# Kernel tuning notes

Measured on AMD Instinct MI355X. Metric: run time of the kernel, lower is better.

## Reference

```python
import jax, jax.numpy as jnp
import numpy as np

EMB = 2048
NQH = 16          # num_q_heads
G = 4             # group_size
NKV = NQH // G    # 4 kv heads
HD = EMB // NQH   # 128 head_dim
B, S = 2, 2048


def setup_inputs() -> dict:
    key = jax.random.key(0)
    ks = jax.random.split(key, 6)
    scale = 1.0 / np.sqrt(EMB)
    x = jax.random.normal(ks[0], (B, S, EMB), dtype=jnp.float32)
    attn_mask = jnp.zeros((B, S), dtype=bool)  # unused placeholder
    # torch Linear weights: (out_features, in_features)
    Wq = jax.random.normal(ks[1], (EMB, EMB), dtype=jnp.float32) * scale
    Wk = jax.random.normal(ks[2], (EMB // G, EMB), dtype=jnp.float32) * scale
    Wv = jax.random.normal(ks[3], (EMB // G, EMB), dtype=jnp.float32) * scale
    Wo = jax.random.normal(ks[4], (EMB, EMB), dtype=jnp.float32) * scale
    return {"x": x, "attn_mask": attn_mask, "is_causal": 1,
            "Wq": Wq, "Wk": Wk, "Wv": Wv, "Wo": Wo}


def reference(x, attn_mask, is_causal, Wq, Wk, Wv, Wo):
    b, n, _ = x.shape
    q = x @ Wq.T                      # (b, n, EMB)
    k = x @ Wk.T                      # (b, n, EMB//G)
    v = x @ Wv.T                      # (b, n, EMB//G)
    # q: b n (h_full d) -> b h_full n d, then (h g) split with h=NKV outer
    q = q.reshape(b, n, NQH, HD).transpose(0, 2, 1, 3)      # (b, NQH, n, d)
    q = q.reshape(b, NKV, G, n, HD).transpose(0, 2, 1, 3, 4)  # (b, g, h, n, d)
    k = k.reshape(b, n, NKV, HD).transpose(0, 2, 1, 3)      # (b, h, s, d)
    v = v.reshape(b, n, NKV, HD).transpose(0, 2, 1, 3)      # (b, h, s, d)
    attn = jnp.einsum('bghnd,bhsd->bghns', q, k) / np.sqrt(HD)
    scores = jax.nn.softmax(attn, axis=-1)  # dropout p=0.0 -> identity
    out = jnp.einsum('bghns,bhsd->bghnd', scores, v)        # (b, g, h, n, d)
    # b g h n d -> b n (h g) d -> b n (h g d)
    out = out.transpose(0, 3, 2, 1, 4).reshape(b, n, EMB)
    y = out @ Wo.T
    return y
```

## Files before the change

kernel.cpp:

```cpp
#include <hip/hip_runtime.h>
#include <stdint.h>


typedef short s8v __attribute__((ext_vector_type(8)));
typedef float f4  __attribute__((ext_vector_type(4)));
typedef unsigned short u16;

#define GLD_LDS(g, l) __builtin_amdgcn_global_load_lds(                     \
    (const __attribute__((address_space(1))) void*)(g),                     \
    (__attribute__((address_space(3))) void*)(l), 16, 0, 0)

__device__ __forceinline__ u16 f2bf(float f) {
    union { float f; uint32_t u; } v; v.f = f;
    uint32_t u = v.u;
    return (u16)((u + 0x7fffu + ((u >> 16) & 1u)) >> 16);
}

__device__ __forceinline__ float fexp2(float x) {
#if __has_builtin(__builtin_amdgcn_exp2f)
    return __builtin_amdgcn_exp2f(x);
#else
    return exp2f(x);
#endif
}

__global__ void cvt_all(const float* __restrict__ x,  const float* __restrict__ wq,
                        const float* __restrict__ wk, const float* __restrict__ wv,
                        const float* __restrict__ wo_,
                        u16* __restrict__ xb, u16* __restrict__ wqkv,
                        u16* __restrict__ wob)
{
    int i = blockIdx.x * blockDim.x + threadIdx.x;
    const float4* s; ushort4* d; int so, dofs;
    if (i < 2097152)      { s = (const float4*)x;   d = (ushort4*)xb;   so = i;           dofs = so; }
    else if (i < 3145728) { s = (const float4*)wq;  d = (ushort4*)wqkv; so = i - 2097152; dofs = so; }
    else if (i < 3407872) { s = (const float4*)wk;  d = (ushort4*)wqkv; so = i - 3145728; dofs = so + 1048576; }
    else if (i < 3670016) { s = (const float4*)wv;  d = (ushort4*)wqkv; so = i - 3407872; dofs = so + 1310720; }
    else                  { s = (const float4*)wo_; d = (ushort4*)wob;  so = i - 3670016; dofs = so; }
    float4 v = s[so];
    ushort4 o;
    o.x = f2bf(v.x); o.y = f2bf(v.y); o.z = f2bf(v.z); o.w = f2bf(v.w);
    d[dofs] = o;
}

__global__ __launch_bounds__(512, 1)
void gemm256x192(const u16* __restrict__ A, const u16* __restrict__ Bm,
                 int K,
                 u16* __restrict__ qkOut, u16* __restrict__ vtOut)
{
    __shared__ __attribute__((aligned(16))) u16 ldsA[2][2][8192];
    __shared__ __attribute__((aligned(16))) u16 ldsB[2][12288];

    const int tid  = threadIdx.x;
    const int lane = tid & 63, quad = lane >> 4, l16 = lane & 15;
    const int wave = tid >> 6;
    const int wr = wave >> 2, wc = wave & 3;

    int bx, by;
    {
        const int nwgx = gridDim.x;
        const int nwg  = nwgx * gridDim.y;
        const int flat = blockIdx.y * nwgx + blockIdx.x;
        const int nflat = (flat & 7) * (nwg >> 3) + (flat >> 3);
        bx = nflat % nwgx; by = nflat / nwgx;
    }
    const int m0 = by * 256, n0 = bx * 192;
    const int NT = K >> 6;

    f4 acc[8][3] = {};

#define VMC3() asm volatile("s_waitcnt vmcnt(3)" ::: "memory")
#define VMC0() asm volatile("s_waitcnt vmcnt(0)" ::: "memory")
#define BAR()  __builtin_amdgcn_s_barrier()

#define STGA(bf, h, t) if ((t) < NT) {                                      \
        _Pragma("unroll")                                                   \
        for (int j = 0; j < 2; j++) {                                       \
            int s_ = j * 512 + tid;                                         \
            int r_ = s_ >> 3, cc = s_ & 7;                                  \
            GLD_LDS(A + (size_t)(m0 + (h) * 128 + r_) * K + (t) * 64        \
                      + ((cc ^ (r_ & 7)) << 3),                             \
                    &ldsA[bf][h][(j * 512 + (tid & ~63)) * 8]);             \
        } }

#define STGB(bf, t) if ((t) < NT) {                                         \
        _Pragma("unroll")                                                   \
        for (int j = 0; j < 3; j++) {                                       \
            int s_ = j * 512 + tid;                                         \
            int r_ = s_ >> 3, cc = s_ & 7;                                  \
            GLD_LDS(Bm + (size_t)(n0 + r_) * K + (t) * 64                   \
                       + ((cc ^ (r_ & 7)) << 3),                            \
                    &ldsB[bf][(j * 512 + (tid & ~63)) * 8]);                \
        } }

#define RD_A(bf, qm, ar) {                                                  \
        _Pragma("unroll")                                                   \
        for (int f = 0; f < 4; f++) {                                       \
            int r_ = (qm) * 64 + f * 16 + l16;                              \
            _Pragma("unroll")                                               \
            for (int kc = 0; kc < 2; kc++)                                  \
                ar[f][kc] = *(const s8v*)(&ldsA[bf][wr]                     \
                    [r_ * 64 + (((kc * 4 + quad) ^ (r_ & 7)) << 3)]);       \
        } }

#define RD_B(bf, br) {                                                      \
        _Pragma("unroll")                                                   \
        for (int f = 0; f < 3; f++) {                                       \
            int r_ = wc * 48 + f * 16 + l16;                                \
            _Pragma("unroll")                                               \
            for (int kc = 0; kc < 2; kc++)                                  \
                br[f][kc] = *(const s8v*)(&ldsB[bf]                         \
                    [r_ * 64 + (((kc * 4 + quad) ^ (r_ & 7)) << 3)]);       \
        } }

#define MM(qm, ar, br) {                                                    \
        __builtin_amdgcn_s_setprio(1);                                      \
        _Pragma("unroll")                                                   \
        for (int f = 0; f < 4; f++)                                         \
            _Pragma("unroll")                                               \
            for (int g = 0; g < 3; g++) {                                   \
                acc[(qm)*4+f][g] = __builtin_amdgcn_mfma_f32_16x16x32_bf16( \
                    ar[f][0], br[g][0], acc[(qm)*4+f][g], 0, 0, 0);         \
                acc[(qm)*4+f][g] = __builtin_amdgcn_mfma_f32_16x16x32_bf16( \
                    ar[f][1], br[g][1], acc[(qm)*4+f][g], 0, 0, 0);         \
            }                                                               \
        __builtin_amdgcn_s_setprio(0); }

    STGA(0,0,0); STGA(0,1,0); STGB(0,0);
    STGB(1,1);
    VMC3(); BAR();

    for (int T = 0; T < NT; T += 2) {
        const bool more = (T + 2 < NT);
        s8v a0[4][2], a1[4][2], b[3][2];
        RD_A(0,0,a0); RD_B(0,b);
        STGA(1,0,T+1); STGA(1,1,T+1);
        BAR(); MM(0,a0,b); BAR();
        RD_A(0,1,a1);
        STGB(0,T+2);
        BAR(); MM(1,a1,b);
        if (more) { VMC3(); } else { VMC0(); }
        BAR();
        RD_A(1,0,a0); RD_B(1,b);
        STGA(0,0,T+2); STGA(0,1,T+2);
        BAR(); MM(0,a0,b); BAR();
        RD_A(1,1,a1);
        STGB(1,T+3);
        BAR(); MM(1,a1,b);
        if (more) { VMC3(); } else { VMC0(); }
        BAR();
    }
#undef STGA
#undef STGB
#undef RD_A
#undef RD_B
#undef MM
#undef VMC3
#undef VMC0
#undef BAR

    const float qs = 0.08838834764831845f * 1.4426950408889634f;
    #pragma unroll
    for (int mi = 0; mi < 8; mi++) {
        int gm0 = m0 + wr * 128 + mi * 16 + quad * 4;
        int bb = gm0 >> 11, s = gm0 & 2047;
        #pragma unroll
        for (int ni = 0; ni < 3; ni++) {
            int base = n0 + wc * 48 + ni * 16;
            int gn = base + l16;
            if (base < 2048) {
                #pragma unroll
                for (int r = 0; r < 4; r++)
                    qkOut[(size_t)(gm0 + r) * 2560 + gn] = f2bf(acc[mi][ni][r] * qs);
            } else if (base < 2560) {
                #pragma unroll
                for (int r = 0; r < 4; r++)
                    qkOut[(size_t)(gm0 + r) * 2560 + gn] = f2bf(acc[mi][ni][r]);
            } else {
                int dd = gn - 2560;
                ushort4 pk;
                pk.x = f2bf(acc[mi][ni][0]); pk.y = f2bf(acc[mi][ni][1]);
                pk.z = f2bf(acc[mi][ni][2]); pk.w = f2bf(acc[mi][ni][3]);
                *(ushort4*)(vtOut +
                    ((size_t)(bb * 4 + (dd >> 7)) * 128 + (dd & 127)) * 2048 + s) = pk;
            }
        }
    }
}

__global__ __launch_bounds__(512, 1)
void gemm256x128(const u16* __restrict__ A, const u16* __restrict__ Bm,
                 int M, int N, int K, float* __restrict__ fOut)
{
    __shared__ __attribute__((aligned(16))) u16 lds[2][3][8192];

    const int tid  = threadIdx.x;
    const int lane = tid & 63, quad = lane >> 4, l16 = lane & 15;
    const int wave = tid >> 6;
    const int wr = wave >> 2, wc = wave & 3;

    int bx, by;
    {
        const int nwgx = gridDim.x;
        const int nwg  = nwgx * gridDim.y;
        const int flat = blockIdx.y * nwgx + blockIdx.x;
        const int nflat = (flat & 7) * (nwg >> 3) + (flat >> 3);
        bx = nflat % nwgx; by = nflat / nwgx;
    }
    const int m0 = by * 256, n0 = bx * 128;
    const int NT = K >> 6;

    f4 acc[8][2] = {};

#define VMC2() asm volatile("s_waitcnt vmcnt(2)" ::: "memory")
#define VMC0() asm volatile("s_waitcnt vmcnt(0)" ::: "memory")
#define BAR()  __builtin_amdgcn_s_barrier()

#define STG(bf, u, t) if ((t) < NT) {                                       \
        const u16* gb = ((u) == 2) ? Bm : A;                                \
        const int rb = ((u) == 2) ? n0 : (m0 + (u) * 128);                  \
        _Pragma("unroll")                                                   \
        for (int j = 0; j < 2; j++) {                                       \
            int s_ = j * 512 + tid;                                         \
            int r_ = s_ >> 3, cc = s_ & 7;                                  \
            GLD_LDS(gb + (size_t)(rb + r_) * K + (t) * 64                   \
                       + ((cc ^ (r_ & 7)) << 3),                            \
                    &lds[bf][u][(j * 512 + (tid & ~63)) * 8]);              \
        } }

#define RD_A(bf, qm, ar) {                                                  \
        _Pragma("unroll")                                                   \
        for (int f = 0; f < 4; f++) {                                       \
            int r_ = (qm) * 64 + f * 16 + l16;                              \
            _Pragma("unroll")                                               \
            for (int kc = 0; kc < 2; kc++)                                  \
                ar[f][kc] = *(const s8v*)(&lds[bf][wr]                      \
                    [r_ * 64 + (((kc * 4 + quad) ^ (r_ & 7)) << 3)]);       \
        } }

#define RD_B(bf, br) {                                                      \
        _Pragma("unroll")                                                   \
        for (int f = 0; f < 2; f++) {                                       \
            int r_ = wc * 32 + f * 16 + l16;                                \
            _Pragma("unroll")                                               \
            for (int kc = 0; kc < 2; kc++)                                  \
                br[f][kc] = *(const s8v*)(&lds[bf][2]                       \
                    [r_ * 64 + (((kc * 4 + quad) ^ (r_ & 7)) << 3)]);       \
        } }

#define MM(qm, ar, br) {                                                    \
        __builtin_amdgcn_s_setprio(1);                                      \
        _Pragma("unroll")                                                   \
        for (int f = 0; f < 4; f++)                                         \
            _Pragma("unroll")                                               \
            for (int g = 0; g < 2; g++) {                                   \
                acc[(qm)*4+f][g] = __builtin_amdgcn_mfma_f32_16x16x32_bf16( \
                    ar[f][0], br[g][0], acc[(qm)*4+f][g], 0, 0, 0);         \
                acc[(qm)*4+f][g] = __builtin_amdgcn_mfma_f32_16x16x32_bf16( \
                    ar[f][1], br[g][1], acc[(qm)*4+f][g], 0, 0, 0);         \
            }                                                               \
        __builtin_amdgcn_s_setprio(0); }

    STG(0,0,0); STG(0,1,0); STG(0,2,0);
    STG(1,2,1);
    VMC2(); BAR();

    for (int T = 0; T < NT; T += 2) {
        const bool more = (T + 2 < NT);
        s8v a0[4][2], a1[4][2], b[2][2];
        RD_A(0,0,a0); RD_B(0,b);
        STG(1,0,T+1); STG(1,1,T+1);
        BAR(); MM(0,a0,b); BAR();
        RD_A(0,1,a1);
        STG(0,2,T+2);
        BAR(); MM(1,a1,b);
        if (more) { VMC2(); } else { VMC0(); }
        BAR();
        RD_A(1,0,a0); RD_B(1,b);
        STG(0,0,T+2); STG(0,1,T+2);
        BAR(); MM(0,a0,b); BAR();
        RD_A(1,1,a1);
        STG(1,2,T+3);
        BAR(); MM(1,a1,b);
        if (more) { VMC2(); } else { VMC0(); }
        BAR();
    }
#undef STG
#undef RD_A
#undef RD_B
#undef MM
#undef VMC2
#undef VMC0
#undef BAR

    #pragma unroll
    for (int mi = 0; mi < 8; mi++) {
        int gm0 = m0 + wr * 128 + mi * 16 + quad * 4;
        #pragma unroll
        for (int ni = 0; ni < 2; ni++) {
            int gn = n0 + wc * 32 + ni * 16 + l16;
            #pragma unroll
            for (int r = 0; r < 4; r++)
                fOut[(size_t)(gm0 + r) * N + gn] = acc[mi][ni][r];
        }
    }
}

__global__ __launch_bounds__(512, 1)
void attn_kernel(const u16* __restrict__ qk, const u16* __restrict__ vt,
                 u16* __restrict__ ao)
{
    __shared__ __attribute__((aligned(16))) u16 Kb[3][64 * 128];
    __shared__ __attribute__((aligned(16))) u16 Vb[3][128 * 64];
    __shared__ __attribute__((aligned(16))) u16 Ps[8][32 * 72];

    const int tid  = threadIdx.x;
    const int wave = tid >> 6, lane = tid & 63;
    const int quad = lane >> 4, l16 = lane & 15;
    const int bh = blockIdx.x;
    const int b = bh >> 2, h = bh & 3;
    const int hh = wave >> 1, mh = wave & 1;
    const int hq = h * 4 + hh;
    const int qs0 = blockIdx.y * 64;

    s8v aq[2][4];
    #pragma unroll
    for (int mt = 0; mt < 2; mt++) {
        const u16* qrow = qk + (size_t)(b * 2048 + qs0 + (mh * 2 + mt) * 16 + l16) * 2560
                             + hq * 128 + quad * 8;
        #pragma unroll
        for (int c4 = 0; c4 < 4; c4++) aq[mt][c4] = *(const s8v*)(qrow + c4 * 32);
    }

    s8v ones;
    #pragma unroll
    for (int j = 0; j < 8; j++) ones[j] = (short)0x3F80;

    f4 o[2][9] = {};

    const u16* kbase = qk + (size_t)(b * 2048) * 2560 + 2048 + h * 128;
    const u16* vbase = vt + (size_t)bh * 128 * 2048;
    u16* Pw = &Ps[wave][0];

    int bkb[4], bvb[2];
    #pragma unroll
    for (int c4 = 0; c4 < 4; c4++)
        bkb[c4] = l16 * 128 + (((c4 * 4 + quad) ^ (l16 & 7)) * 8);
    #pragma unroll
    for (int kc = 0; kc < 2; kc++)
        bvb[kc] = l16 * 64 + (((kc * 4 + quad) ^ (l16 & 7)) * 8);
    const int apb = l16 * 72 + quad * 8;
    const int psw = l16 * 72 + quad * 4;

#define VMC4() asm volatile("s_waitcnt vmcnt(4)" ::: "memory")
#define VMC0() asm volatile("s_waitcnt vmcnt(0)" ::: "memory")

#define STAGE(BUF, S) {                                                       \
        _Pragma("unroll")                                                     \
        for (int i = 0; i < 2; i++) {                                         \
            const int c = wave + i * 8;                                       \
            int kr = c * 4 + (lane >> 4);                                     \
            int ksw = (lane & 15) ^ (kr & 7);                                 \
            GLD_LDS(kbase + (size_t)((S) + kr) * 2560 + ksw * 8,              \
                    &Kb[BUF][c * 512]);                                       \
            int vd = c * 8 + (lane >> 3);                                     \
            int vsw = (lane & 7) ^ (vd & 7);                                  \
            GLD_LDS(vbase + (size_t)vd * 2048 + (S) + vsw * 8,                \
                    &Vb[BUF][c * 512]);                                       \
        } }

#define STEP(CUR, NXT, S) {                                                   \
        if ((S) + 64 < 2048) { VMC4(); } else { VMC0(); }                     \
        __builtin_amdgcn_s_barrier();                                         \
        if ((S) + 128 < 2048) STAGE(NXT, (S) + 128);                          \
        s8v bk[4][4];                                                         \
        _Pragma("unroll")                                                     \
        for (int c4 = 0; c4 < 4; c4++)                                        \
            _Pragma("unroll")                                                 \
            for (int cg = 0; cg < 4; cg++)                                    \
                bk[c4][cg] = *(const s8v*)(&Kb[CUR][bkb[c4] + cg * 2048]);    \
        _Pragma("unroll")                                                     \
        for (int mt = 0; mt < 2; mt++) {                                      \
            f4 sc[4] = {};                                                    \
            _Pragma("unroll")                                                 \
            for (int c4 = 0; c4 < 4; c4++)                                    \
                _Pragma("unroll")                                             \
                for (int cg = 0; cg < 4; cg++)                                \
                    sc[cg] = __builtin_amdgcn_mfma_f32_16x16x32_bf16(         \
                        bk[c4][cg], aq[mt][c4], sc[cg], 0, 0, 0);             \
            _Pragma("unroll")                                                 \
            for (int cg = 0; cg < 4; cg++) {                                  \
                ushort4 pk;                                                   \
                pk.x = (u16)(__float_as_uint(fexp2(sc[cg][0])) >> 16);        \
                pk.y = (u16)(__float_as_uint(fexp2(sc[cg][1])) >> 16);        \
                pk.z = (u16)(__float_as_uint(fexp2(sc[cg][2])) >> 16);        \
                pk.w = (u16)(__float_as_uint(fexp2(sc[cg][3])) >> 16);        \
                *(ushort4*)(Pw + psw + mt * 1152 + cg * 16) = pk;             \
            }                                                                 \
        }                                                                     \
        s8v ap[2][2];                                                         \
        _Pragma("unroll")                                                     \
        for (int mt = 0; mt < 2; mt++)                                        \
            _Pragma("unroll")                                                 \
            for (int kc = 0; kc < 2; kc++)                                    \
                ap[mt][kc] = *(const s8v*)(Pw + apb + mt * 1152 + kc * 32);   \
        _Pragma("unroll")                                                     \
        for (int ch = 0; ch < 8; ch++) {                                      \
            s8v bv0 = *(const s8v*)(&Vb[CUR][bvb[0] + ch * 1024]);            \
            s8v bv1 = *(const s8v*)(&Vb[CUR][bvb[1] + ch * 1024]);            \
            _Pragma("unroll")                                                 \
            for (int mt = 0; mt < 2; mt++) {                                  \
                o[mt][ch] = __builtin_amdgcn_mfma_f32_16x16x32_bf16(          \
                    ap[mt][0], bv0, o[mt][ch], 0, 0, 0);                      \
                o[mt][ch] = __builtin_amdgcn_mfma_f32_16x16x32_bf16(          \
                    ap[mt][1], bv1, o[mt][ch], 0, 0, 0);                      \
            }                                                                 \
        }                                                                     \
        _Pragma("unroll")                                                     \
        for (int mt = 0; mt < 2; mt++) {                                      \
            o[mt][8] = __builtin_amdgcn_mfma_f32_16x16x32_bf16(               \
                ap[mt][0], ones, o[mt][8], 0, 0, 0);                          \
            o[mt][8] = __builtin_amdgcn_mfma_f32_16x16x32_bf16(               \
                ap[mt][1], ones, o[mt][8], 0, 0, 0);                          \
        } }

    STAGE(0, 0);
    STAGE(1, 64);
    int s0 = 0;
    for (int it = 0; it < 10; ++it, s0 += 192) {
        STEP(0, 2, s0);
        STEP(1, 0, s0 + 64);
        STEP(2, 1, s0 + 128);
    }
    STEP(0, 2, 1920);
    STEP(1, 0, 1984);
#undef STEP
#undef STAGE
#undef VMC4
#undef VMC0

    #pragma unroll
    for (int mt = 0; mt < 2; mt++)
        #pragma unroll
        for (int r = 0; r < 4; r++) {
            float inv = 1.f / o[mt][8][r];
            int gm = b * 2048 + qs0 + (mh * 2 + mt) * 16 + quad * 4 + r;
            #pragma unroll
            for (int ch = 0; ch < 8; ch++)
                ao[(size_t)gm * 2048 + hq * 128 + ch * 16 + l16] =
                    f2bf(o[mt][ch][r] * inv);
        }
}

extern "C" void kernel_launch(void* const* d_in, const int* in_sizes, int n_in,
                              void* d_out, int out_size, void* d_ws, size_t ws_size,
                              hipStream_t stream)
{
    const float* x  = (const float*)d_in[0];
    const float* Wq = (const float*)d_in[3];
    const float* Wk = (const float*)d_in[4];
    const float* Wv = (const float*)d_in[5];
    const float* Wo = (const float*)d_in[6];

    char* ws = (char*)d_ws;
    u16* xb   = (u16*)(ws);
    u16* wqkv = (u16*)(ws + 16777216);
    u16* wo   = (u16*)(ws + 29360128);
    u16* qkb  = (u16*)(ws + 37748736);
    u16* vtb  = (u16*)(ws + 58720256);
    u16* ao   = (u16*)(ws + 62914560);
    if (ws_size < 79691776u) return;

    cvt_all<<<18432, 256, 0, stream>>>(x, Wq, Wk, Wv, Wo, xb, wqkv, wo);

    gemm256x192<<<dim3(16, 16), 512, 0, stream>>>(xb, wqkv, 2048, qkb, vtb);
    attn_kernel<<<dim3(8, 32), 512, 0, stream>>>(qkb, vtb, ao);
    gemm256x128<<<dim3(16, 16), 512, 0, stream>>>(ao, wo, 4096, 2048, 2048,
                                                  (float*)d_out);
}
```

Baseline: 268.9 us.

## Software-pipeline attention loop: overlap next tile's QK softmax with current PV

Splits the per-tile attention step into a QK/exp phase and a PV phase, then reorders them so the QK^T, exp and P writeback of tile i+1 are issued before the PV MFMAs of tile i. Two register sets of P fragments alternate across a 6-way unrolled loop with a matching prologue and epilogue. s_setprio is raised around the PV MFMA block to favour matrix-core issue. The load wait changes from vmcnt(4) to vmcnt(0), which shortens the effective prefetch lookahead and adds register pressure from the second P fragment set.

Measured after the change: 274.5 us. 2.1% more time.

```diff
diff --git a/kernel.cpp b/kernel.cpp
--- a/kernel.cpp
+++ b/kernel.cpp
@@ -354,6 +354,7 @@
 
 #define VMC4() asm volatile("s_waitcnt vmcnt(4)" ::: "memory")
 #define VMC0() asm volatile("s_waitcnt vmcnt(0)" ::: "memory")
+#define BARR() __builtin_amdgcn_s_barrier()
 
 #define STAGE(BUF, S) {                                                       \
         _Pragma("unroll")                                                     \
@@ -369,16 +370,13 @@
                     &Vb[BUF][c * 512]);                                       \
         } }
 
-#define STEP(CUR, NXT, S) {                                                   \
-        if ((S) + 64 < 2048) { VMC4(); } else { VMC0(); }                     \
-        __builtin_amdgcn_s_barrier();                                         \
-        if ((S) + 128 < 2048) STAGE(NXT, (S) + 128);                          \
+#define QKPH(KB, ap) {                                                        \
         s8v bk[4][4];                                                         \
         _Pragma("unroll")                                                     \
         for (int c4 = 0; c4 < 4; c4++)                                        \
             _Pragma("unroll")                                                 \
             for (int cg = 0; cg < 4; cg++)                                    \
-                bk[c4][cg] = *(const s8v*)(&Kb[CUR][bkb[c4] + cg * 2048]);    \
+                bk[c4][cg] = *(const s8v*)(&Kb[KB][bkb[c4] + cg * 2048]);     \
         _Pragma("unroll")                                                     \
         for (int mt = 0; mt < 2; mt++) {                                      \
             f4 sc[4] = {};                                                    \
@@ -398,16 +396,18 @@
                 *(ushort4*)(Pw + psw + mt * 1152 + cg * 16) = pk;             \
             }                                                                 \
         }                                                                     \
-        s8v ap[2][2];                                                         \
         _Pragma("unroll")                                                     \
         for (int mt = 0; mt < 2; mt++)                                        \
             _Pragma("unroll")                                                 \
             for (int kc = 0; kc < 2; kc++)                                    \
-                ap[mt][kc] = *(const s8v*)(Pw + apb + mt * 1152 + kc * 32);   \
+                ap[mt][kc] = *(const s8v*)(Pw + apb + mt * 1152 + kc * 32);   }
+
+#define PVPH(VB, ap) {                                                        \
+        __builtin_amdgcn_s_setprio(1);                                        \
         _Pragma("unroll")                                                     \
         for (int ch = 0; ch < 8; ch++) {                                      \
-            s8v bv0 = *(const s8v*)(&Vb[CUR][bvb[0] + ch * 1024]);            \
-            s8v bv1 = *(const s8v*)(&Vb[CUR][bvb[1] + ch * 1024]);            \
+            s8v bv0 = *(const s8v*)(&Vb[VB][bvb[0] + ch * 1024]);             \
+            s8v bv1 = *(const s8v*)(&Vb[VB][bvb[1] + ch * 1024]);             \
             _Pragma("unroll")                                                 \
             for (int mt = 0; mt < 2; mt++) {                                  \
                 o[mt][ch] = __builtin_amdgcn_mfma_f32_16x16x32_bf16(          \
@@ -422,22 +422,40 @@
                 ap[mt][0], ones, o[mt][8], 0, 0, 0);                          \
             o[mt][8] = __builtin_amdgcn_mfma_f32_16x16x32_bf16(               \
                 ap[mt][1], ones, o[mt][8], 0, 0, 0);                          \
-        } }
+        }                                                                     \
+        __builtin_amdgcn_s_setprio(0); }
+
+    s8v apA[2][2], apB[2][2];
 
     STAGE(0, 0);
     STAGE(1, 64);
+    VMC4(); BARR();
+    QKPH(0, apA);
+
     int s0 = 0;
-    for (int it = 0; it < 10; ++it, s0 += 192) {
-        STEP(0, 2, s0);
-        STEP(1, 0, s0 + 64);
-        STEP(2, 1, s0 + 128);
-    }
-    STEP(0, 2, 1920);
-    STEP(1, 0, 1984);
-#undef STEP
+    for (int it = 0; it < 5; ++it, s0 += 384) {
+        VMC0(); BARR(); STAGE(2, s0 + 128);
+        QKPH(1, apB); PVPH(0, apA);
+        VMC0(); BARR(); STAGE(0, s0 + 192);
+        QKPH(2, apA); PVPH(1, apB);
+        VMC0(); BARR(); STAGE(1, s0 + 256);
+        QKPH(0, apB); PVPH(2, apA);
+        VMC0(); BARR(); STAGE(2, s0 + 320);
+        QKPH(1, apA); PVPH(0, apB);
+        VMC0(); BARR(); STAGE(0, s0 + 384);
+        QKPH(2, apB); PVPH(1, apA);
+        VMC0(); BARR(); if (s0 + 448 < 2048) STAGE(1, s0 + 448);
+        QKPH(0, apA); PVPH(2, apB);
+    }
+    VMC0(); BARR();
+    QKPH(1, apB); PVPH(0, apA);
+    PVPH(1, apB);
+#undef QKPH
+#undef PVPH
 #undef STAGE
 #undef VMC4
 #undef VMC0
+#undef BARR
 
     #pragma unroll
     for (int mt = 0; mt < 2; mt++)
```

## Split attention work per wave by key half and output-dim half, share P across wave pairs

Applied to the files above, without the earlier changes.

Each wave now handles all 64 query rows of its head, computes scores against half of the 64-key tile, and writes them into a P buffer shared by the wave pair. After a barrier, each wave multiplies the full P by half of the V head dimension. K and V fragments are loaded once per wave and reused across four query tiles instead of two, cutting LDS reads per MFMA. The cost is an extra block-wide barrier per step, a redundant row-sum MFMA in both waves, and higher register pressure from the doubled Q fragments. An s_setprio hint is also placed around the PV MFMA section.

Result: no change. 268.2 us (-0.3%).

```diff
diff --git a/kernel.cpp b/kernel.cpp
--- a/kernel.cpp
+++ b/kernel.cpp
@@ -312,21 +312,21 @@
 {
     __shared__ __attribute__((aligned(16))) u16 Kb[3][64 * 128];
     __shared__ __attribute__((aligned(16))) u16 Vb[3][128 * 64];
-    __shared__ __attribute__((aligned(16))) u16 Ps[8][32 * 72];
+    __shared__ __attribute__((aligned(16))) u16 Ps[4][64 * 72];
 
     const int tid  = threadIdx.x;
     const int wave = tid >> 6, lane = tid & 63;
     const int quad = lane >> 4, l16 = lane & 15;
     const int bh = blockIdx.x;
     const int b = bh >> 2, h = bh & 3;
-    const int hh = wave >> 1, mh = wave & 1;
+    const int hh = wave >> 1, half = wave & 1;
     const int hq = h * 4 + hh;
     const int qs0 = blockIdx.y * 64;
 
-    s8v aq[2][4];
-    #pragma unroll
-    for (int mt = 0; mt < 2; mt++) {
-        const u16* qrow = qk + (size_t)(b * 2048 + qs0 + (mh * 2 + mt) * 16 + l16) * 2560
+    s8v aq[4][4];
+    #pragma unroll
+    for (int mt = 0; mt < 4; mt++) {
+        const u16* qrow = qk + (size_t)(b * 2048 + qs0 + mt * 16 + l16) * 2560
                              + hq * 128 + quad * 8;
         #pragma unroll
         for (int c4 = 0; c4 < 4; c4++) aq[mt][c4] = *(const s8v*)(qrow + c4 * 32);
@@ -336,21 +336,22 @@
     #pragma unroll
     for (int j = 0; j < 8; j++) ones[j] = (short)0x3F80;
 
-    f4 o[2][9] = {};
+    f4 o[4][5] = {};
 
     const u16* kbase = qk + (size_t)(b * 2048) * 2560 + 2048 + h * 128;
     const u16* vbase = vt + (size_t)bh * 128 * 2048;
-    u16* Pw = &Ps[wave][0];
-
-    int bkb[4], bvb[2];
+    u16* Pw = &Ps[hh][0];
+
+    int bkb[4];
     #pragma unroll
     for (int c4 = 0; c4 < 4; c4++)
-        bkb[c4] = l16 * 128 + (((c4 * 4 + quad) ^ (l16 & 7)) * 8);
+        bkb[c4] = l16 * 128 + (((c4 * 4 + quad) ^ (l16 & 7)) * 8) + half * 4096;
+    int bvb[2];
     #pragma unroll
     for (int kc = 0; kc < 2; kc++)
         bvb[kc] = l16 * 64 + (((kc * 4 + quad) ^ (l16 & 7)) * 8);
     const int apb = l16 * 72 + quad * 8;
-    const int psw = l16 * 72 + quad * 4;
+    const int psw = l16 * 72 + half * 32 + quad * 4;
 
 #define VMC4() asm volatile("s_waitcnt vmcnt(4)" ::: "memory")
 #define VMC0() asm volatile("s_waitcnt vmcnt(0)" ::: "memory")
@@ -373,56 +374,64 @@
         if ((S) + 64 < 2048) { VMC4(); } else { VMC0(); }                     \
         __builtin_amdgcn_s_barrier();                                         \
         if ((S) + 128 < 2048) STAGE(NXT, (S) + 128);                          \
-        s8v bk[4][4];                                                         \
+                                          \
+        {                                                                     \
+            f4 sc[4][2] = {};                                                 \
+            _Pragma("unroll")                                                 \
+            for (int c4 = 0; c4 < 4; c4++) {                                  \
+                s8v bk0 = *(const s8v*)(&Kb[CUR][bkb[c4]]);                   \
+                s8v bk1 = *(const s8v*)(&Kb[CUR][bkb[c4] + 2048]);            \
+                _Pragma("unroll")                                             \
+                for (int mt = 0; mt < 4; mt++) {                              \
+                    sc[mt][0] = __builtin_amdgcn_mfma_f32_16x16x32_bf16(      \
+                        bk0, aq[mt][c4], sc[mt][0], 0, 0, 0);                 \
+                    sc[mt][1] = __builtin_amdgcn_mfma_f32_16x16x32_bf16(      \
+                        bk1, aq[mt][c4], sc[mt][1], 0, 0, 0);                 \
+                }                                                             \
+            }                                                                 \
+            _Pragma("unroll")                                                 \
+            for (int mt = 0; mt < 4; mt++)                                    \
+                _Pragma("unroll")                                             \
+                for (int g = 0; g < 2; g++) {                                 \
+                    ushort4 pk;                                               \
+                    pk.x = (u16)(__float_as_uint(fexp2(sc[mt][g][0])) >> 16); \
+                    pk.y = (u16)(__float_as_uint(fexp2(sc[mt][g][1])) >> 16); \
+                    pk.z = (u16)(__float_as_uint(fexp2(sc[mt][g][2])) >> 16); \
+                    pk.w = (u16)(__float_as_uint(fexp2(sc[mt][g][3])) >> 16); \
+                    *(ushort4*)(Pw + psw + mt * 1152 + g * 16) = pk;          \
+                }                                                             \
+        }                                                                     \
+        asm volatile("s_waitcnt lgkmcnt(0)" ::: "memory");                    \
+        __builtin_amdgcn_s_barrier();          \
+                                   \
+        s8v ap[4][2];                                                         \
         _Pragma("unroll")                                                     \
-        for (int c4 = 0; c4 < 4; c4++)                                        \
-            _Pragma("unroll")                                                 \
-            for (int cg = 0; cg < 4; cg++)                                    \
-                bk[c4][cg] = *(const s8v*)(&Kb[CUR][bkb[c4] + cg * 2048]);    \
-        _Pragma("unroll")                                                     \
-        for (int mt = 0; mt < 2; mt++) {                                      \
-            f4 sc[4] = {};                                                    \
-            _Pragma("unroll")                                                 \
-            for (int c4 = 0; c4 < 4; c4++)                                    \
-                _Pragma("unroll")                                             \
-                for (int cg = 0; cg < 4; cg++)                                \
-                    sc[cg] = __builtin_amdgcn_mfma_f32_16x16x32_bf16(         \
-                        bk[c4][cg], aq[mt][c4], sc[cg], 0, 0, 0);             \
-            _Pragma("unroll")                                                 \
-            for (int cg = 0; cg < 4; cg++) {                                  \
-                ushort4 pk;                                                   \
-                pk.x = (u16)(__float_as_uint(fexp2(sc[cg][0])) >> 16);        \
-                pk.y = (u16)(__float_as_uint(fexp2(sc[cg][1])) >> 16);        \
-                pk.z = (u16)(__float_as_uint(fexp2(sc[cg][2])) >> 16);        \
-                pk.w = (u16)(__float_as_uint(fexp2(sc[cg][3])) >> 16);        \
-                *(ushort4*)(Pw + psw + mt * 1152 + cg * 16) = pk;             \
-            }                                                                 \
-        }                                                                     \
-        s8v ap[2][2];                                                         \
-        _Pragma("unroll")                                                     \
-        for (int mt = 0; mt < 2; mt++)                                        \
+        for (int mt = 0; mt < 4; mt++)                                        \
             _Pragma("unroll")                                                 \
             for (int kc = 0; kc < 2; kc++)                                    \
                 ap[mt][kc] = *(const s8v*)(Pw + apb + mt * 1152 + kc * 32);   \
+        __builtin_amdgcn_s_setprio(1);                                        \
         _Pragma("unroll")                                                     \
-        for (int ch = 0; ch < 8; ch++) {                                      \
+        for (int chl = 0; chl < 4; chl++) {                                   \
+            const int ch = half * 4 + chl;                                    \
             s8v bv0 = *(const s8v*)(&Vb[CUR][bvb[0] + ch * 1024]);            \
             s8v bv1 = *(const s8v*)(&Vb[CUR][bvb[1] + ch * 1024]);            \
             _Pragma("unroll")                                                 \
-            for (int mt = 0; mt < 2; mt++) {                                  \
-                o[mt][ch] = __builtin_amdgcn_mfma_f32_16x16x32_bf16(          \
-                    ap[mt][0], bv0, o[mt][ch], 0, 0, 0);                      \
-                o[mt][ch] = __builtin_amdgcn_mfma_f32_16x16x32_bf16(          \
-                    ap[mt][1], bv1, o[mt][ch], 0, 0, 0);                      \
+            for (int mt = 0; mt < 4; mt++) {                                  \
+                o[mt][chl] = __builtin_amdgcn_mfma_f32_16x16x32_bf16(         \
+                    ap[mt][0], bv0, o[mt][chl], 0, 0, 0);                     \
+                o[mt][chl] = __builtin_amdgcn_mfma_f32_16x16x32_bf16(         \
+                    ap[mt][1], bv1, o[mt][chl], 0, 0, 0);                     \
             }                                                                 \
         }                                                                     \
         _Pragma("unroll")                                                     \
-        for (int mt = 0; mt < 2; mt++) {                                      \
-            o[mt][8] = __builtin_amdgcn_mfma_f32_16x16x32_bf16(               \
-                ap[mt][0], ones, o[mt][8], 0, 0, 0);                          \
-            o[mt][8] = __builtin_amdgcn_mfma_f32_16x16x32_bf16(               \
-                ap[mt][1], ones, o[mt][8], 0, 0, 0);                          \
-        } }
+        for (int mt = 0; mt < 4; mt++) {                                      \
+            o[mt][4] = __builtin_amdgcn_mfma_f32_16x16x32_bf16(               \
+                ap[mt][0], ones, o[mt][4], 0, 0, 0);                          \
+            o[mt][4] = __builtin_amdgcn_mfma_f32_16x16x32_bf16(               \
+                ap[mt][1], ones, o[mt][4], 0, 0, 0);                          \
+        }                                                                     \
+        __builtin_amdgcn_s_setprio(0); }
 
     STAGE(0, 0);
     STAGE(1, 64);
@@ -440,15 +449,15 @@
 #undef VMC0
 
     #pragma unroll
-    for (int mt = 0; mt < 2; mt++)
+    for (int mt = 0; mt < 4; mt++)
         #pragma unroll
         for (int r = 0; r < 4; r++) {
-            float inv = 1.f / o[mt][8][r];
-            int gm = b * 2048 + qs0 + (mh * 2 + mt) * 16 + quad * 4 + r;
+            float inv = 1.f / o[mt][4][r];
+            int gm = b * 2048 + qs0 + mt * 16 + quad * 4 + r;
             #pragma unroll
-            for (int ch = 0; ch < 8; ch++)
-                ao[(size_t)gm * 2048 + hq * 128 + ch * 16 + l16] =
-                    f2bf(o[mt][ch][r] * inv);
+            for (int chl = 0; chl < 4; chl++)
+                ao[(size_t)gm * 2048 + hq * 128 + (half * 4 + chl) * 16 + l16] =
+                    f2bf(o[mt][chl][r] * inv);
         }
 }
 
```
